# Kernel tuning notes

Hardware: AMD Instinct MI355X
Metric: run time of the kernel (lower is better)

## Reference

```python
import jax, jax.numpy as jnp
import numpy as np

N_NODES = 50000
IN_DIM = 128
HIDDEN = 64
N_EDGES = 1600000


def setup_inputs() -> dict:
    key = jax.random.key(0)
    k1, k2, k3, k4, k5, k6 = jax.random.split(key, 6)
    x_proj = jax.random.normal(k1, (N_NODES, IN_DIM), dtype=jnp.float32)
    edge_index = jax.random.randint(k2, (2, N_EDGES), 0, N_NODES, dtype=jnp.int64)
    # Linear(2*in_dim, hidden): PyTorch stores weight as [out, in]; keep that layout.
    lim1 = 1.0 / np.sqrt(2 * IN_DIM)
    w1 = jax.random.uniform(k3, (HIDDEN, 2 * IN_DIM), minval=-lim1, maxval=lim1, dtype=jnp.float32)
    b1 = jax.random.uniform(k4, (HIDDEN,), minval=-lim1, maxval=lim1, dtype=jnp.float32)
    lim2 = 1.0 / np.sqrt(HIDDEN)
    w2 = jax.random.uniform(k5, (1, HIDDEN), minval=-lim2, maxval=lim2, dtype=jnp.float32)
    b2 = jax.random.uniform(k6, (1,), minval=-lim2, maxval=lim2, dtype=jnp.float32)
    return {"x_proj": x_proj, "edge_index": edge_index, "w1": w1, "b1": b1, "w2": w2, "b2": b2}


def reference(x_proj, edge_index, w1, b1, w2, b2):
    # Chunking in the original is only for memory; math == single vectorized pass.
    row, col = edge_index[0], edge_index[1]
    h = jnp.concatenate([x_proj[row], x_proj[col]], axis=1)  # [E, 2*in_dim]
    h = jax.nn.relu(h @ w1.T + b1)                            # [E, hidden]
    s = jax.nn.sigmoid(h @ w2.T + b2).squeeze(-1)             # [E]
    return s
```

## Files before the change

### kernel.cpp

```cpp
#include <hip/hip_runtime.h>
#include <hip/hip_bf16.h>


typedef __attribute__((ext_vector_type(8))) short bf16x8;
typedef __attribute__((ext_vector_type(4))) float f32x4;
typedef __attribute__((ext_vector_type(4))) int   i32x4;

#define IN_DIM 128
#define HIDDEN 64
#define QSCALE (2.5f / 127.0f)
#define QINV   (127.0f / 2.5f)

__device__ __forceinline__ unsigned short bfbits(float f) {
    __hip_bfloat16 h = __float2bfloat16(f);
    return __builtin_bit_cast(unsigned short, h);
}

__device__ __forceinline__ bf16x8 pack8(const float4& lo, const float4& hi) {
    bf16x8 b;
    b[0] = (short)bfbits(lo.x); b[1] = (short)bfbits(lo.y);
    b[2] = (short)bfbits(lo.z); b[3] = (short)bfbits(lo.w);
    b[4] = (short)bfbits(hi.x); b[5] = (short)bfbits(hi.y);
    b[6] = (short)bfbits(hi.z); b[7] = (short)bfbits(hi.w);
    return b;
}

__global__ __launch_bounds__(256) void node_proj_kernel(
    const float* __restrict__ x,
    const float* __restrict__ w1,
    const float* __restrict__ b1,
    unsigned char* __restrict__ itab,
    int N, int ntiles)
{
    __shared__ short wfrag[2048 * 8];

    {
        int v = threadIdx.x;
#pragma unroll
        for (int j = 0; j < 8; ++j) {
            int f = v * 64 + j * 8;
            int r = f >> 8;
            int k = f & 255;
            float4 lo = *(const float4*)(w1 + f);
            float4 hi = *(const float4*)(w1 + f + 4);
            int o, kk, g;
            if (k < IN_DIM) { o = r;          kk = k >> 5;             g = (k & 31) >> 3; }
            else            { o = r + HIDDEN; kk = (k - IN_DIM) >> 5;  g = ((k - IN_DIM) & 31) >> 3; }
            int dt = o >> 4, m = o & 15;
            int lane = g * 16 + m;
            *(bf16x8*)&wfrag[((dt * 4 + kk) * 64 + lane) * 8] = pack8(lo, hi);
        }
    }
    __syncthreads();

    int wave = (int)((blockIdx.x * blockDim.x + threadIdx.x) >> 6);
    if (wave >= ntiles) return;

    int lane = threadIdx.x & 63;
    int m = lane & 15;
    int g = lane >> 4;
    int n0 = wave * 16;

    int node = n0 + m;
    bool valid = node < N;
    int nc = valid ? node : N - 1;
    const float* xr = x + (size_t)nc * IN_DIM;

    bf16x8 xf[4];
#pragma unroll
    for (int kk = 0; kk < 4; ++kk) {
        int k0 = kk * 32 + g * 8;
        float4 lo = *(const float4*)(xr + k0);
        float4 hi = *(const float4*)(xr + k0 + 4);
        xf[kk] = pack8(lo, hi);
    }

    f32x4 acc[8] = {};
#pragma unroll
    for (int dt = 0; dt < 8; ++dt) {
#pragma unroll
        for (int kk = 0; kk < 4; ++kk) {
            bf16x8 wf = *(const bf16x8*)&wfrag[((dt * 4 + kk) * 64 + lane) * 8];
            acc[dt] = __builtin_amdgcn_mfma_f32_16x16x32_bf16(wf, xf[kk], acc[dt], 0, 0, 0);
        }
    }

#pragma unroll
    for (int dt = 0; dt < 4; ++dt) {
        float4 b4 = *(const float4*)(b1 + dt * 16 + g * 4);
        acc[dt][0] += b4.x; acc[dt][1] += b4.y;
        acc[dt][2] += b4.z; acc[dt][3] += b4.w;
    }

    if (valid) {
        unsigned char* irow = itab + (size_t)node * 128;
#pragma unroll
        for (int dt = 0; dt < 8; ++dt) {
            unsigned w = 0;
#pragma unroll
            for (int r = 0; r < 4; ++r) {
                float v = rintf(acc[dt][r] * QINV);
                v = fminf(fmaxf(v, -128.f), 127.f);
                int qv = (int)v;
                w |= ((unsigned)(qv + 128) & 0xffu) << (8 * r);
            }
            *(unsigned*)(irow + dt * 16 + g * 4) = w;
        }
    }
}

__device__ __forceinline__ float quad_i8(unsigned a, unsigned b, const float4& w, float acc) {
    float u;
    u = (float)(a & 0xffu)         + (float)(b & 0xffu);
    acc = fmaf(fmaxf(u, 256.f), w.x, acc);
    u = (float)((a >> 8) & 0xffu)  + (float)((b >> 8) & 0xffu);
    acc = fmaf(fmaxf(u, 256.f), w.y, acc);
    u = (float)((a >> 16) & 0xffu) + (float)((b >> 16) & 0xffu);
    acc = fmaf(fmaxf(u, 256.f), w.z, acc);
    u = (float)(a >> 24)           + (float)(b >> 24);
    acc = fmaf(fmaxf(u, 256.f), w.w, acc);
    return acc;
}

__device__ __forceinline__ float edge_dot4(const uint4& qa, const uint4& qb,
                                           const float4& w0, const float4& w1v,
                                           const float4& w2v, const float4& w3,
                                           float Wl) {
    float acc = 0.f;
    acc = quad_i8(qa.x, qb.x, w0, acc);
    acc = quad_i8(qa.y, qb.y, w1v, acc);
    acc = quad_i8(qa.z, qb.z, w2v, acc);
    acc = quad_i8(qa.w, qb.w, w3, acc);
    float part = fmaf(-256.f, Wl, acc);
    part += __shfl_xor(part, 1);
    part += __shfl_xor(part, 2);
    return part;
}

__device__ __forceinline__ float sigmoidf(float z) {
    return 1.f / (1.f + __expf(-z));
}

__global__ __launch_bounds__(256) void edge_kernel(
    const int* __restrict__ ei,
    const unsigned char* __restrict__ itab,
    const float* __restrict__ w2,
    const float* __restrict__ b2,
    float* __restrict__ out,
    int E)
{
    int t = (int)(blockIdx.x * 256 + threadIdx.x);
    int q = t >> 2;
    int sub = t & 3;
    long long e0 = (long long)q * 8;
    if (e0 >= E) return;

    int so = sub << 4;
    float4 w0  = *((const float4*)w2 + sub * 4 + 0);
    float4 w1v = *((const float4*)w2 + sub * 4 + 1);
    float4 w2v = *((const float4*)w2 + sub * 4 + 2);
    float4 w3  = *((const float4*)w2 + sub * 4 + 3);
    float Wl = (w0.x + w0.y + w0.z + w0.w) + (w1v.x + w1v.y + w1v.z + w1v.w)
             + (w2v.x + w2v.y + w2v.z + w2v.w) + (w3.x + w3.y + w3.z + w3.w);

    if (e0 + 8 <= E) {
        i32x4 ra = __builtin_nontemporal_load((const i32x4*)(ei + e0));
        i32x4 rb = __builtin_nontemporal_load((const i32x4*)(ei + e0 + 4));
        i32x4 ca = __builtin_nontemporal_load((const i32x4*)(ei + E + e0));
        i32x4 cb = __builtin_nontemporal_load((const i32x4*)(ei + E + e0 + 4));
        uint4 a0 = *(const uint4*)(itab + ((size_t)ra[0] << 7) + so);
        uint4 a1 = *(const uint4*)(itab + ((size_t)ra[1] << 7) + so);
        uint4 a2 = *(const uint4*)(itab + ((size_t)ra[2] << 7) + so);
        uint4 a3 = *(const uint4*)(itab + ((size_t)ra[3] << 7) + so);
        uint4 a4 = *(const uint4*)(itab + ((size_t)rb[0] << 7) + so);
        uint4 a5 = *(const uint4*)(itab + ((size_t)rb[1] << 7) + so);
        uint4 a6 = *(const uint4*)(itab + ((size_t)rb[2] << 7) + so);
        uint4 a7 = *(const uint4*)(itab + ((size_t)rb[3] << 7) + so);
        uint4 c0 = *(const uint4*)(itab + ((size_t)ca[0] << 7) + 64 + so);
        uint4 c1 = *(const uint4*)(itab + ((size_t)ca[1] << 7) + 64 + so);
        uint4 c2 = *(const uint4*)(itab + ((size_t)ca[2] << 7) + 64 + so);
        uint4 c3 = *(const uint4*)(itab + ((size_t)ca[3] << 7) + 64 + so);
        uint4 c4 = *(const uint4*)(itab + ((size_t)cb[0] << 7) + 64 + so);
        uint4 c5 = *(const uint4*)(itab + ((size_t)cb[1] << 7) + 64 + so);
        uint4 c6 = *(const uint4*)(itab + ((size_t)cb[2] << 7) + 64 + so);
        uint4 c7 = *(const uint4*)(itab + ((size_t)cb[3] << 7) + 64 + so);

        float z0 = edge_dot4(a0, c0, w0, w1v, w2v, w3, Wl);
        float z1 = edge_dot4(a1, c1, w0, w1v, w2v, w3, Wl);
        float z2 = edge_dot4(a2, c2, w0, w1v, w2v, w3, Wl);
        float z3 = edge_dot4(a3, c3, w0, w1v, w2v, w3, Wl);
        float z4 = edge_dot4(a4, c4, w0, w1v, w2v, w3, Wl);
        float z5 = edge_dot4(a5, c5, w0, w1v, w2v, w3, Wl);
        float z6 = edge_dot4(a6, c6, w0, w1v, w2v, w3, Wl);
        float z7 = edge_dot4(a7, c7, w0, w1v, w2v, w3, Wl);

        if (sub == 0) {
            float bb = b2[0];
            f32x4 s0, s1;
            s0[0] = sigmoidf(fmaf(QSCALE, z0, bb));
            s0[1] = sigmoidf(fmaf(QSCALE, z1, bb));
            s0[2] = sigmoidf(fmaf(QSCALE, z2, bb));
            s0[3] = sigmoidf(fmaf(QSCALE, z3, bb));
            s1[0] = sigmoidf(fmaf(QSCALE, z4, bb));
            s1[1] = sigmoidf(fmaf(QSCALE, z5, bb));
            s1[2] = sigmoidf(fmaf(QSCALE, z6, bb));
            s1[3] = sigmoidf(fmaf(QSCALE, z7, bb));
            __builtin_nontemporal_store(s0, (f32x4*)(out + e0));
            __builtin_nontemporal_store(s1, (f32x4*)(out + e0 + 4));
        }
    } else {
        float bb = b2[0];
        for (long long e = e0; e < E; ++e) {
            int row = ei[e];
            int col = ei[E + e];
            uint4 ua = *(const uint4*)(itab + ((size_t)row << 7) + so);
            uint4 ub = *(const uint4*)(itab + ((size_t)col << 7) + 64 + so);
            float z = edge_dot4(ua, ub, w0, w1v, w2v, w3, Wl);
            if (sub == 0) out[e] = sigmoidf(fmaf(QSCALE, z, bb));
        }
    }
}

extern "C" void kernel_launch(void* const* d_in, const int* in_sizes, int n_in,
                              void* d_out, int out_size, void* d_ws, size_t ws_size,
                              hipStream_t stream) {
    const float* x  = (const float*)d_in[0];
    const int*   ei = (const int*)d_in[1];
    const float* w1 = (const float*)d_in[2];
    const float* b1 = (const float*)d_in[3];
    const float* w2 = (const float*)d_in[4];
    const float* b2 = (const float*)d_in[5];
    float* out = (float*)d_out;

    int N = in_sizes[0] / IN_DIM;
    int E = in_sizes[1] / 2;

    unsigned char* itab = (unsigned char*)d_ws;

    int ntiles = (N + 15) / 16;
    int nblocks = (ntiles + 3) / 4;
    node_proj_kernel<<<nblocks, 256, 0, stream>>>(x, w1, b1, itab, N, ntiles);

    long long groups = ((long long)E + 7) / 8;
    long long tthreads = groups * 4;
    int eblocks = (int)((tthreads + 255) / 256);
    edge_kernel<<<eblocks, 256, 0, stream>>>(ei, itab, w2, b2, out, E);
}
```

Measured before the change: 52.90 us.

## Fuse node projection and edge scoring into one cooperative persistent kernel

Merges the node-projection and edge kernels into a single cooperative launch. A persistent grid loops over node tiles, synchronizes across the whole grid, then processes edge groups with a grid-stride loop, which removes the second kernel launch and its inter-kernel gap. The costs are a grid-wide barrier, a capped grid size that may reduce latency hiding for the gather-heavy edge phase, and a hard-coded CU count of 256 in the sizing. If the cooperative launch fails, it falls back to the two-kernel path.

```diff
diff --git a/kernel.cpp b/kernel.cpp
--- a/kernel.cpp
+++ b/kernel.cpp
@@ -1,5 +1,8 @@
 #include <hip/hip_runtime.h>
 #include <hip/hip_bf16.h>
+#include <hip/hip_cooperative_groups.h>
+
+namespace cg = cooperative_groups;
 
 
 typedef __attribute__((ext_vector_type(8))) short bf16x8;
@@ -25,86 +28,81 @@
     return b;
 }
 
-__global__ __launch_bounds__(256) void node_proj_kernel(
-    const float* __restrict__ x,
-    const float* __restrict__ w1,
-    const float* __restrict__ b1,
-    unsigned char* __restrict__ itab,
-    int N, int ntiles)
-{
-    __shared__ short wfrag[2048 * 8];
-
-    {
-        int v = threadIdx.x;
-#pragma unroll
-        for (int j = 0; j < 8; ++j) {
-            int f = v * 64 + j * 8;
-            int r = f >> 8;
-            int k = f & 255;
-            float4 lo = *(const float4*)(w1 + f);
-            float4 hi = *(const float4*)(w1 + f + 4);
-            int o, kk, g;
-            if (k < IN_DIM) { o = r;          kk = k >> 5;             g = (k & 31) >> 3; }
-            else            { o = r + HIDDEN; kk = (k - IN_DIM) >> 5;  g = ((k - IN_DIM) & 31) >> 3; }
-            int dt = o >> 4, m = o & 15;
-            int lane = g * 16 + m;
-            *(bf16x8*)&wfrag[((dt * 4 + kk) * 64 + lane) * 8] = pack8(lo, hi);
-        }
-    }
-    __syncthreads();
-
-    int wave = (int)((blockIdx.x * blockDim.x + threadIdx.x) >> 6);
-    if (wave >= ntiles) return;
-
+
+__device__ __forceinline__ void stage_w1(const float* __restrict__ w1, short* wfrag) {
+    int v = threadIdx.x;
+#pragma unroll
+    for (int j = 0; j < 8; ++j) {
+        int f = v * 64 + j * 8;
+        int r = f >> 8;
+        int k = f & 255;
+        float4 lo = *(const float4*)(w1 + f);
+        float4 hi = *(const float4*)(w1 + f + 4);
+        int o, kk, g;
+        if (k < IN_DIM) { o = r;          kk = k >> 5;             g = (k & 31) >> 3; }
+        else            { o = r + HIDDEN; kk = (k - IN_DIM) >> 5;  g = ((k - IN_DIM) & 31) >> 3; }
+        int dt = o >> 4, m = o & 15;
+        int lane = g * 16 + m;
+        *(bf16x8*)&wfrag[((dt * 4 + kk) * 64 + lane) * 8] = pack8(lo, hi);
+    }
+}
+
+__device__ __forceinline__ void node_phase(
+    const float* __restrict__ x, const float* __restrict__ b1,
+    const short* wfrag, unsigned char* __restrict__ itab,
+    int N, int ntiles, int gwave, int wstride)
+{
     int lane = threadIdx.x & 63;
     int m = lane & 15;
     int g = lane >> 4;
-    int n0 = wave * 16;
-
-    int node = n0 + m;
-    bool valid = node < N;
-    int nc = valid ? node : N - 1;
-    const float* xr = x + (size_t)nc * IN_DIM;
-
-    bf16x8 xf[4];
-#pragma unroll
-    for (int kk = 0; kk < 4; ++kk) {
-        int k0 = kk * 32 + g * 8;
-        float4 lo = *(const float4*)(xr + k0);
-        float4 hi = *(const float4*)(xr + k0 + 4);
-        xf[kk] = pack8(lo, hi);
-    }
-
-    f32x4 acc[8] = {};
-#pragma unroll
-    for (int dt = 0; dt < 8; ++dt) {
+
+    for (int t = gwave; t < ntiles; t += wstride) {
+        int n0 = t * 16;
+        int node = n0 + m;
+        bool valid = node < N;
+        int nc = valid ? node : N - 1;
+        const float* xr = x + (size_t)nc * IN_DIM;
+
+        bf16x8 xf[4];
 #pragma unroll
         for (int kk = 0; kk < 4; ++kk) {
-            bf16x8 wf = *(const bf16x8*)&wfrag[((dt * 4 + kk) * 64 + lane) * 8];
-            acc[dt] = __builtin_amdgcn_mfma_f32_16x16x32_bf16(wf, xf[kk], acc[dt], 0, 0, 0);
-        }
-    }
-
-#pragma unroll
-    for (int dt = 0; dt < 4; ++dt) {
-        float4 b4 = *(const float4*)(b1 + dt * 16 + g * 4);
-        acc[dt][0] += b4.x; acc[dt][1] += b4.y;
-        acc[dt][2] += b4.z; acc[dt][3] += b4.w;
-    }
-
-    if (valid) {
-        unsigned char* irow = itab + (size_t)node * 128;
+            int k0 = kk * 32 + g * 8;
+            float4 lo = *(const float4*)(xr + k0);
+            float4 hi = *(const float4*)(xr + k0 + 4);
+            xf[kk] = pack8(lo, hi);
+        }
+
+        f32x4 acc[8] = {};
 #pragma unroll
         for (int dt = 0; dt < 8; ++dt) {
-            unsigned w = 0;
-#pragma unroll
-            for (int r = 0; r < 4; ++r) {
-                float v = rintf(acc[dt][r] * QINV);
-                v = fminf(fmaxf(v, -128.f), 127.f);
-                int qv = (int)v;
-                w |= ((unsigned)(qv + 128) & 0xffu) << (8 * r);
-            }
-            *(unsigned*)(irow + dt * 16 + g * 4) = w;
+#pragma unroll
+            for (int kk = 0; kk < 4; ++kk) {
+                bf16x8 wf = *(const bf16x8*)&wfrag[((dt * 4 + kk) * 64 + lane) * 8];
+                acc[dt] = __builtin_amdgcn_mfma_f32_16x16x32_bf16(wf, xf[kk], acc[dt], 0, 0, 0);
+            }
+        }
+
+#pragma unroll
+        for (int dt = 0; dt < 4; ++dt) {
+            float4 b4 = *(const float4*)(b1 + dt * 16 + g * 4);
+            acc[dt][0] += b4.x; acc[dt][1] += b4.y;
+            acc[dt][2] += b4.z; acc[dt][3] += b4.w;
+        }
+
+        if (valid) {
+            unsigned char* irow = itab + (size_t)node * 128;
+#pragma unroll
+            for (int dt = 0; dt < 8; ++dt) {
+                unsigned w = 0;
+#pragma unroll
+                for (int r = 0; r < 4; ++r) {
+                    float v = rintf(acc[dt][r] * QINV);
+                    v = fminf(fmaxf(v, -128.f), 127.f);
+                    int qv = (int)v;
+                    w |= ((unsigned)(qv + 128) & 0xffu) << (8 * r);
+                }
+                *(unsigned*)(irow + dt * 16 + g * 4) = w;
+            }
         }
     }
 }
@@ -141,20 +139,12 @@
     return 1.f / (1.f + __expf(-z));
 }
 
-__global__ __launch_bounds__(256) void edge_kernel(
-    const int* __restrict__ ei,
-    const unsigned char* __restrict__ itab,
-    const float* __restrict__ w2,
-    const float* __restrict__ b2,
-    float* __restrict__ out,
-    int E)
-{
-    int t = (int)(blockIdx.x * 256 + threadIdx.x);
-    int q = t >> 2;
-    int sub = t & 3;
-    long long e0 = (long long)q * 8;
-    if (e0 >= E) return;
-
+__device__ __forceinline__ void edge_phase(
+    const int* __restrict__ ei, const unsigned char* __restrict__ itab,
+    const float* __restrict__ w2, const float* __restrict__ b2,
+    float* __restrict__ out, int E, long long grp0, long long gstep)
+{
+    int sub = threadIdx.x & 3;
     int so = sub << 4;
     float4 w0  = *((const float4*)w2 + sub * 4 + 0);
     float4 w1v = *((const float4*)w2 + sub * 4 + 1);
@@ -162,63 +152,107 @@
     float4 w3  = *((const float4*)w2 + sub * 4 + 3);
     float Wl = (w0.x + w0.y + w0.z + w0.w) + (w1v.x + w1v.y + w1v.z + w1v.w)
              + (w2v.x + w2v.y + w2v.z + w2v.w) + (w3.x + w3.y + w3.z + w3.w);
-
-    if (e0 + 8 <= E) {
-        i32x4 ra = __builtin_nontemporal_load((const i32x4*)(ei + e0));
-        i32x4 rb = __builtin_nontemporal_load((const i32x4*)(ei + e0 + 4));
-        i32x4 ca = __builtin_nontemporal_load((const i32x4*)(ei + E + e0));
-        i32x4 cb = __builtin_nontemporal_load((const i32x4*)(ei + E + e0 + 4));
-        uint4 a0 = *(const uint4*)(itab + ((size_t)ra[0] << 7) + so);
-        uint4 a1 = *(const uint4*)(itab + ((size_t)ra[1] << 7) + so);
-        uint4 a2 = *(const uint4*)(itab + ((size_t)ra[2] << 7) + so);
-        uint4 a3 = *(const uint4*)(itab + ((size_t)ra[3] << 7) + so);
-        uint4 a4 = *(const uint4*)(itab + ((size_t)rb[0] << 7) + so);
-        uint4 a5 = *(const uint4*)(itab + ((size_t)rb[1] << 7) + so);
-        uint4 a6 = *(const uint4*)(itab + ((size_t)rb[2] << 7) + so);
-        uint4 a7 = *(const uint4*)(itab + ((size_t)rb[3] << 7) + so);
-        uint4 c0 = *(const uint4*)(itab + ((size_t)ca[0] << 7) + 64 + so);
-        uint4 c1 = *(const uint4*)(itab + ((size_t)ca[1] << 7) + 64 + so);
-        uint4 c2 = *(const uint4*)(itab + ((size_t)ca[2] << 7) + 64 + so);
-        uint4 c3 = *(const uint4*)(itab + ((size_t)ca[3] << 7) + 64 + so);
-        uint4 c4 = *(const uint4*)(itab + ((size_t)cb[0] << 7) + 64 + so);
-        uint4 c5 = *(const uint4*)(itab + ((size_t)cb[1] << 7) + 64 + so);
-        uint4 c6 = *(const uint4*)(itab + ((size_t)cb[2] << 7) + 64 + so);
-        uint4 c7 = *(const uint4*)(itab + ((size_t)cb[3] << 7) + 64 + so);
-
-        float z0 = edge_dot4(a0, c0, w0, w1v, w2v, w3, Wl);
-        float z1 = edge_dot4(a1, c1, w0, w1v, w2v, w3, Wl);
-        float z2 = edge_dot4(a2, c2, w0, w1v, w2v, w3, Wl);
-        float z3 = edge_dot4(a3, c3, w0, w1v, w2v, w3, Wl);
-        float z4 = edge_dot4(a4, c4, w0, w1v, w2v, w3, Wl);
-        float z5 = edge_dot4(a5, c5, w0, w1v, w2v, w3, Wl);
-        float z6 = edge_dot4(a6, c6, w0, w1v, w2v, w3, Wl);
-        float z7 = edge_dot4(a7, c7, w0, w1v, w2v, w3, Wl);
-
-        if (sub == 0) {
-            float bb = b2[0];
-            f32x4 s0, s1;
-            s0[0] = sigmoidf(fmaf(QSCALE, z0, bb));
-            s0[1] = sigmoidf(fmaf(QSCALE, z1, bb));
-            s0[2] = sigmoidf(fmaf(QSCALE, z2, bb));
-            s0[3] = sigmoidf(fmaf(QSCALE, z3, bb));
-            s1[0] = sigmoidf(fmaf(QSCALE, z4, bb));
-            s1[1] = sigmoidf(fmaf(QSCALE, z5, bb));
-            s1[2] = sigmoidf(fmaf(QSCALE, z6, bb));
-            s1[3] = sigmoidf(fmaf(QSCALE, z7, bb));
-            __builtin_nontemporal_store(s0, (f32x4*)(out + e0));
-            __builtin_nontemporal_store(s1, (f32x4*)(out + e0 + 4));
-        }
-    } else {
-        float bb = b2[0];
-        for (long long e = e0; e < E; ++e) {
-            int row = ei[e];
-            int col = ei[E + e];
-            uint4 ua = *(const uint4*)(itab + ((size_t)row << 7) + so);
-            uint4 ub = *(const uint4*)(itab + ((size_t)col << 7) + 64 + so);
-            float z = edge_dot4(ua, ub, w0, w1v, w2v, w3, Wl);
-            if (sub == 0) out[e] = sigmoidf(fmaf(QSCALE, z, bb));
-        }
-    }
+    float bb = b2[0];
+
+    for (long long grp = grp0; grp * 8 < E; grp += gstep) {
+        long long e0 = grp * 8;
+        if (e0 + 8 <= E) {
+            i32x4 ra = __builtin_nontemporal_load((const i32x4*)(ei + e0));
+            i32x4 rb = __builtin_nontemporal_load((const i32x4*)(ei + e0 + 4));
+            i32x4 ca = __builtin_nontemporal_load((const i32x4*)(ei + E + e0));
+            i32x4 cb = __builtin_nontemporal_load((const i32x4*)(ei + E + e0 + 4));
+            uint4 a0 = *(const uint4*)(itab + ((size_t)ra[0] << 7) + so);
+            uint4 a1 = *(const uint4*)(itab + ((size_t)ra[1] << 7) + so);
+            uint4 a2 = *(const uint4*)(itab + ((size_t)ra[2] << 7) + so);
+            uint4 a3 = *(const uint4*)(itab + ((size_t)ra[3] << 7) + so);
+            uint4 a4 = *(const uint4*)(itab + ((size_t)rb[0] << 7) + so);
+            uint4 a5 = *(const uint4*)(itab + ((size_t)rb[1] << 7) + so);
+            uint4 a6 = *(const uint4*)(itab + ((size_t)rb[2] << 7) + so);
+            uint4 a7 = *(const uint4*)(itab + ((size_t)rb[3] << 7) + so);
+            uint4 c0 = *(const uint4*)(itab + ((size_t)ca[0] << 7) + 64 + so);
+            uint4 c1 = *(const uint4*)(itab + ((size_t)ca[1] << 7) + 64 + so);
+            uint4 c2 = *(const uint4*)(itab + ((size_t)ca[2] << 7) + 64 + so);
+            uint4 c3 = *(const uint4*)(itab + ((size_t)ca[3] << 7) + 64 + so);
+            uint4 c4 = *(const uint4*)(itab + ((size_t)cb[0] << 7) + 64 + so);
+            uint4 c5 = *(const uint4*)(itab + ((size_t)cb[1] << 7) + 64 + so);
+            uint4 c6 = *(const uint4*)(itab + ((size_t)cb[2] << 7) + 64 + so);
+            uint4 c7 = *(const uint4*)(itab + ((size_t)cb[3] << 7) + 64 + so);
+
+            float z0 = edge_dot4(a0, c0, w0, w1v, w2v, w3, Wl);
+            float z1 = edge_dot4(a1, c1, w0, w1v, w2v, w3, Wl);
+            float z2 = edge_dot4(a2, c2, w0, w1v, w2v, w3, Wl);
+            float z3 = edge_dot4(a3, c3, w0, w1v, w2v, w3, Wl);
+            float z4 = edge_dot4(a4, c4, w0, w1v, w2v, w3, Wl);
+            float z5 = edge_dot4(a5, c5, w0, w1v, w2v, w3, Wl);
+            float z6 = edge_dot4(a6, c6, w0, w1v, w2v, w3, Wl);
+            float z7 = edge_dot4(a7, c7, w0, w1v, w2v, w3, Wl);
+
+            if (sub == 0) {
+                f32x4 s0, s1;
+                s0[0] = sigmoidf(fmaf(QSCALE, z0, bb));
+                s0[1] = sigmoidf(fmaf(QSCALE, z1, bb));
+                s0[2] = sigmoidf(fmaf(QSCALE, z2, bb));
+                s0[3] = sigmoidf(fmaf(QSCALE, z3, bb));
+                s1[0] = sigmoidf(fmaf(QSCALE, z4, bb));
+                s1[1] = sigmoidf(fmaf(QSCALE, z5, bb));
+                s1[2] = sigmoidf(fmaf(QSCALE, z6, bb));
+                s1[3] = sigmoidf(fmaf(QSCALE, z7, bb));
+                __builtin_nontemporal_store(s0, (f32x4*)(out + e0));
+                __builtin_nontemporal_store(s1, (f32x4*)(out + e0 + 4));
+            }
+        } else {
+            for (long long e = e0; e < E; ++e) {
+                int row = ei[e];
+                int col = ei[E + e];
+                uint4 ua = *(const uint4*)(itab + ((size_t)row << 7) + so);
+                uint4 ub = *(const uint4*)(itab + ((size_t)col << 7) + 64 + so);
+                float z = edge_dot4(ua, ub, w0, w1v, w2v, w3, Wl);
+                if (sub == 0) out[e] = sigmoidf(fmaf(QSCALE, z, bb));
+            }
+        }
+    }
+}
+
+
+__global__ __launch_bounds__(256) void fused_kernel(
+    const float* __restrict__ x, const int* __restrict__ ei,
+    const float* __restrict__ w1, const float* __restrict__ b1,
+    const float* __restrict__ w2, const float* __restrict__ b2,
+    float* __restrict__ out, unsigned char* __restrict__ itab,
+    int N, int E, int ntiles)
+{
+    __shared__ short wfrag[2048 * 8];
+    stage_w1(w1, wfrag);
+    __syncthreads();
+
+    int gwave = (int)blockIdx.x * 4 + ((int)threadIdx.x >> 6);
+    node_phase(x, b1, wfrag, itab, N, ntiles, gwave, (int)gridDim.x * 4);
+
+    cg::this_grid().sync();
+
+    long long grp0 = (long long)blockIdx.x * 64 + (threadIdx.x >> 2);
+    edge_phase(ei, itab, w2, b2, out, E, grp0, (long long)gridDim.x * 64);
+}
+
+__global__ __launch_bounds__(256) void node_proj_kernel(
+    const float* __restrict__ x, const float* __restrict__ w1,
+    const float* __restrict__ b1, unsigned char* __restrict__ itab,
+    int N, int ntiles)
+{
+    __shared__ short wfrag[2048 * 8];
+    stage_w1(w1, wfrag);
+    __syncthreads();
+    int gwave = (int)blockIdx.x * 4 + ((int)threadIdx.x >> 6);
+    node_phase(x, b1, wfrag, itab, N, ntiles, gwave, (int)gridDim.x * 4);
+}
+
+__global__ __launch_bounds__(256) void edge_kernel(
+    const int* __restrict__ ei, const unsigned char* __restrict__ itab,
+    const float* __restrict__ w2, const float* __restrict__ b2,
+    float* __restrict__ out, int E)
+{
+    long long grp0 = (long long)blockIdx.x * 64 + (threadIdx.x >> 2);
+    edge_phase(ei, itab, w2, b2, out, E, grp0, (long long)gridDim.x * 64);
 }
 
 extern "C" void kernel_launch(void* const* d_in, const int* in_sizes, int n_in,
@@ -234,15 +268,30 @@
 
     int N = in_sizes[0] / IN_DIM;
     int E = in_sizes[1] / 2;
+    int ntiles = (N + 15) / 16;
 
     unsigned char* itab = (unsigned char*)d_ws;
 
-    int ntiles = (N + 15) / 16;
-    int nblocks = (ntiles + 3) / 4;
-    node_proj_kernel<<<nblocks, 256, 0, stream>>>(x, w1, b1, itab, N, ntiles);
-
-    long long groups = ((long long)E + 7) / 8;
-    long long tthreads = groups * 4;
-    int eblocks = (int)((tthreads + 255) / 256);
-    edge_kernel<<<eblocks, 256, 0, stream>>>(ei, itab, w2, b2, out, E);
-}
+    hipError_t lerr = hipErrorUnknown;
+    int blocksPerCU = 0;
+    hipError_t oerr = hipOccupancyMaxActiveBlocksPerMultiprocessor(
+        &blocksPerCU, (const void*)fused_kernel, 256, 0);
+    if (oerr == hipSuccess && blocksPerCU > 0) {
+        long long maxco = (long long)blocksPerCU * 256;
+        int grid = (int)(maxco < 2048 ? maxco : 2048);
+        void* args[] = {
+            (void*)&x, (void*)&ei, (void*)&w1, (void*)&b1, (void*)&w2, (void*)&b2,
+            (void*)&out, (void*)&itab, (void*)&N, (void*)&E, (void*)&ntiles
+        };
+        lerr = hipLaunchCooperativeKernel((const void*)fused_kernel,
+                                          dim3(grid), dim3(256), args, 0, stream);
+    }
+
+    if (lerr != hipSuccess) {
+        int nblocks = (ntiles + 3) / 4;
+        node_proj_kernel<<<nblocks, 256, 0, stream>>>(x, w1, b1, itab, N, ntiles);
+        long long groups = ((long long)E + 7) / 8;
+        int eblocks = (int)((groups + 63) / 64);
+        edge_kernel<<<eblocks, 256, 0, stream>>>(ei, itab, w2, b2, out, E);
+    }
+}
```

Measured after the change: 99.40 us. +87.9%, slower.
